# Kernel optimization log

Hardware: AMD Instinct MI355X
Metric: run time of the kernel (lower is better)

The kernel has to match this reference:

```python
import jax, jax.numpy as jnp
import numpy as np

# ---- static config (mirrors PointRend init kwargs) ----
H, W = 512, 512          # img_size
CH, CW = 128, 128        # coarse_size
FH, FW = 256, 256        # fine_size
CF = 256                 # fine_channels
NC = 3                   # num_classes (forced by MLP's hard-coded 259/131 channel counts)
NPTS = 2048              # N points
K_OVER = 3               # k oversampling
BELTA = 0.75
NUM_OVER = K_OVER * NPTS          # 6144
STEP1 = int(NPTS * BELTA)         # 1536 uncertain points
STEP2 = NPTS - STEP1              # 512 coverage points


def _xavier(key, c_out, c_in):
    std = (2.0 / (c_in + c_out)) ** 0.5
    return jax.random.normal(key, (c_out, c_in), jnp.float32) * std


def setup_inputs() -> dict:
    key = jax.random.key(0)
    k1, k2, k3, k4, k5, k6 = jax.random.split(key, 6)
    fine_grained = jax.random.normal(k1, (2, CF, FH, FW), jnp.float32)
    coarse_pre = jax.random.normal(k2, (2, NC, CH, CW), jnp.float32)
    # torch.randperm(H*W) done inside forward in the original; passed in for determinism
    random_1d_index = jax.random.permutation(k3, H * W).astype(jnp.int32)
    w1 = _xavier(k4, 256, CF + NC)   # conv1: 1x1, in=259, out=256, no bias
    w2 = _xavier(k5, 128, 256 + 3)   # conv2: in=259, out=128
    w3 = _xavier(k6, NC, 128 + 3)    # conv3: in=131, out=num_classes
    prelu_a = jnp.array(0.25, jnp.float32)  # shared single-param PReLU
    return dict(fine_grained=fine_grained, coarse_pre=coarse_pre,
                w1=w1, w2=w2, w3=w3, prelu_a=prelu_a,
                random_1d_index=random_1d_index)


def _bilinear(x, h, w):
    # matches nn.Upsample(mode='bilinear', align_corners=False)
    return jax.image.resize(x, (x.shape[0], x.shape[1], h, w), method="bilinear")


def _prelu(x, a):
    return jnp.where(x >= 0, x, a * x)


def _mlp(feat, w1, w2, w3, a):
    # feat: [B, N, C] -> channels-first [B, C, N]; BatchNorms in MLP are unused in forward.
    x = jnp.transpose(feat, (0, 2, 1))
    tail = x[:, -3:, :]  # last 3 channels appended to each layer's input
    l1 = _prelu(jnp.einsum('bcn,oc->bon', x, w1), a)
    l2 = _prelu(jnp.einsum('bcn,oc->bon', jnp.concatenate([l1, tail], 1), w2), a)
    return jnp.einsum('bcn,oc->bon', jnp.concatenate([l2, tail], 1), w3)  # [B, NC, N]


def reference(fine_grained, coarse_pre, w1, w2, w3, prelu_a, random_1d_index):
    B = fine_grained.shape[0]
    up_coarse_o = _bilinear(coarse_pre, H, W)            # [B, NC, H, W] logits
    up_coarse_sm = jax.nn.softmax(up_coarse_o, axis=1)   # softmax over classes
    up_fine = _bilinear(fine_grained, H, W)              # [B, CF, H, W]

    h_idx = random_1d_index // W
    w_idx = random_1d_index % W
    all_index = jnp.stack([h_idx, w_idx], axis=1)        # [H*W, 2]
    cand = all_index[:NUM_OVER]                          # oversampled candidates

    # vectorized replacement of the python loop: gather probs at candidates
    over_pre = up_coarse_sm[:, :, cand[:, 0], cand[:, 1]].transpose(0, 2, 1)  # [B, NUM_OVER, NC]
    top2, _ = jax.lax.top_k(over_pre, 2)
    uncertain = 1.0 - (top2[..., 0] - top2[..., 1])      # [B, NUM_OVER]
    _, u_idx = jax.lax.top_k(uncertain, STEP1)           # [B, STEP1]
    u_pts = cand[u_idx]                                  # [B, STEP1, 2]
    cov = jnp.broadcast_to(all_index[-STEP2:][None], (B, STEP2, 2))
    pts = jnp.concatenate([u_pts, cov], axis=1)          # [B, N, 2]

    # masked_select traverses the dense mask in row-major (h,w) order -> sort linear ids
    lin = pts[..., 0] * W + pts[..., 1]                  # [B, N]
    lin_sorted = jnp.sort(lin, axis=1)
    sh, sw = lin_sorted // W, lin_sorted % W
    bidx = jnp.arange(B)[:, None]
    sel_coarse = up_coarse_o[bidx, :, sh, sw]            # [B, N, NC] (pre-softmax feats)
    sel_fine = up_fine[bidx, :, sh, sw]                  # [B, N, CF]

    # faithful to torch: flat concat of the two masked_select outputs, then reshape
    feat = jnp.concatenate([sel_fine.reshape(-1), sel_coarse.reshape(-1)]).reshape(B, NPTS, -1)

    out = _mlp(feat, w1, w2, w3, prelu_a)                # [B, NC, N]
    mask = jnp.zeros((B, H, W), jnp.int32).at[bidx, pts[..., 0], pts[..., 1]].add(1)
    return out, mask
```

## Files before the change

### kernel.cpp

```cpp
#include <hip/hip_runtime.h>

#define NPTS 2048
#define NOVER 6144
#define STEP1 1536
#define STEP2 512
#define HW_TOT 262144

__device__ __forceinline__ float prelu_f(float x, float a) { return x >= 0.0f ? x : a * x; }

__device__ __forceinline__ void coarse_coords(int h, int w, float& fy, float& fx,
                                              int& y0, int& y1, int& x0, int& x1) {
  float sy = (h + 0.5f) * 0.25f - 0.5f;
  float sx = (w + 0.5f) * 0.25f - 0.5f;
  float yf = floorf(sy), xf = floorf(sx);
  fy = sy - yf; fx = sx - xf;
  int yi = (int)yf, xi = (int)xf;
  y0 = min(127, max(0, yi)); y1 = min(127, max(0, yi + 1));
  x0 = min(127, max(0, xi)); x1 = min(127, max(0, xi + 1));
}

__device__ __forceinline__ float coarse_sample(const float* __restrict__ ch, float fy, float fx,
                                               int y0, int y1, int x0, int x1) {
  float v00 = ch[(y0 << 7) + x0];
  float v01 = ch[(y0 << 7) + x1];
  float v10 = ch[(y1 << 7) + x0];
  float v11 = ch[(y1 << 7) + x1];
  return (1.0f - fy) * ((1.0f - fx) * v00 + fx * v01) + fy * ((1.0f - fx) * v10 + fx * v11);
}

__global__ __launch_bounds__(256) void pr_fill_v4(uint4* __restrict__ p) {
  p[blockIdx.x * 256 + threadIdx.x] = make_uint4(0u, 0u, 0u, 0u);
}

__global__ __launch_bounds__(256) void pr_wprep_v4(const float* __restrict__ w1,
                                                   const float* __restrict__ w2,
                                                   float* __restrict__ wT1,
                                                   float* __restrict__ wT2) {
  int gid = blockIdx.x * 256 + threadIdx.x;
  if (gid < 259 * 256) {
    int c = gid >> 8, o = gid & 255;
    wT1[c * 256 + o] = w1[o * 259 + c];
  } else {
    int g2 = gid - 259 * 256;
    if (g2 < 259 * 128) {
      int c = g2 >> 7, o = g2 & 127;
      wT2[c * 128 + o] = w2[o * 259 + c];
    }
  }
}

__global__ __launch_bounds__(256) void pr_uncert_v4(const float* __restrict__ coarse,
                                                    const int* __restrict__ ridx,
                                                    unsigned* __restrict__ keys) {
  int gid = blockIdx.x * 256 + threadIdx.x;
  if (gid >= 2 * NOVER) return;
  int b = gid / NOVER, i = gid - b * NOVER;
  int lin = ridx[i];
  int h = lin >> 9, w = lin & 511;
  float fy, fx; int y0, y1, x0, x1;
  coarse_coords(h, w, fy, fx, y0, y1, x0, x1);
  const float* cb = coarse + (((size_t)b * 3) << 14);
  float p0 = coarse_sample(cb, fy, fx, y0, y1, x0, x1);
  float p1 = coarse_sample(cb + (1 << 14), fy, fx, y0, y1, x0, x1);
  float p2 = coarse_sample(cb + (2 << 14), fy, fx, y0, y1, x0, x1);
  float m = fmaxf(p0, fmaxf(p1, p2));
  float e0 = expf(p0 - m), e1 = expf(p1 - m), e2 = expf(p2 - m);
  float s = e0 + e1 + e2;
  float q0 = e0 / s, q1 = e1 / s, q2 = e2 / s;
  float a0 = q0, a1 = q1, a2 = q2, tmp;
  if (a0 < a1) { tmp = a0; a0 = a1; a1 = tmp; }
  if (a1 < a2) { tmp = a1; a1 = a2; a2 = tmp; }
  if (a0 < a1) { tmp = a0; a0 = a1; a1 = tmp; }
  float u = 1.0f - (a0 - a1);
  keys[gid] = __float_as_uint(u);
}

__global__ __launch_bounds__(1024) void pr_topk_v4(const unsigned* __restrict__ keys,
                                                   const int* __restrict__ ridx,
                                                   int* __restrict__ lin_sorted,
                                                   float* __restrict__ mask) {
  __shared__ unsigned kv[NOVER];
  __shared__ unsigned bitmap[8192];
  __shared__ unsigned hist[256];
  __shared__ unsigned short tiebuf[NOVER];
  __shared__ unsigned scanbuf[16];
  __shared__ unsigned selinfo[2];
  __shared__ int tiecnt;
  const int b = blockIdx.x, t = threadIdx.x;
  const int lane = t & 63, wid = t >> 6;

  for (int i = t; i < NOVER; i += 1024) kv[i] = keys[b * NOVER + i];
  for (int i = t; i < 8192; i += 1024) bitmap[i] = 0u;
  if (t == 0) { selinfo[1] = STEP1; tiecnt = 0; }
  __syncthreads();

  unsigned prefix = 0u;
  for (int pass = 0; pass < 4; ++pass) {
    const int shift = 24 - 8 * pass;
    const unsigned maskHi = (pass == 0) ? 0u : (0xFFFFFFFFu << (shift + 8));
    for (int i = t; i < 256; i += 1024) hist[i] = 0u;
    __syncthreads();
    for (int i = t; i < NOVER; i += 1024) {
      unsigned k = kv[i];
      if ((k & maskHi) == prefix) atomicAdd(&hist[(k >> shift) & 255u], 1u);
    }
    __syncthreads();
    if (t < 64) {
      unsigned h0 = hist[t * 4], h1 = hist[t * 4 + 1], h2 = hist[t * 4 + 2], h3 = hist[t * 4 + 3];
      unsigned q = h0 + h1 + h2 + h3;
      unsigned s = q;
      for (int off = 1; off < 64; off <<= 1) {
        unsigned n = __shfl_down(s, off);
        if (t + off < 64) s += n;
      }
      unsigned exq = s - q;
      unsigned R = selinfo[1];
      unsigned se3 = exq, se2 = se3 + h3, se1 = se2 + h2, se0 = se1 + h1;
      if (se3 < R && R <= se3 + h3)      { selinfo[0] = prefix | ((unsigned)(t * 4 + 3) << shift); selinfo[1] = R - se3; }
      else if (se2 < R && R <= se2 + h2) { selinfo[0] = prefix | ((unsigned)(t * 4 + 2) << shift); selinfo[1] = R - se2; }
      else if (se1 < R && R <= se1 + h1) { selinfo[0] = prefix | ((unsigned)(t * 4 + 1) << shift); selinfo[1] = R - se1; }
      else if (se0 < R && R <= se0 + h0) { selinfo[0] = prefix | ((unsigned)(t * 4 + 0) << shift); selinfo[1] = R - se0; }
    }
    __syncthreads();
    prefix = selinfo[0];
  }
  const unsigned T = prefix;
  const int r = (int)selinfo[1];

  for (int i = t; i < NOVER; i += 1024) {
    unsigned k = kv[i];
    if (k > T) {
      int lin = ridx[i];
      mask[(size_t)b * HW_TOT + lin] = 1.0f;
      atomicOr(&bitmap[lin >> 5], 1u << (lin & 31));
    } else if (k == T) {
      int pos = atomicAdd(&tiecnt, 1);
      tiebuf[pos] = (unsigned short)i;
    }
  }
  for (int i = t; i < STEP2; i += 1024) {
    int lin = ridx[HW_TOT - STEP2 + i];
    mask[(size_t)b * HW_TOT + lin] = 1.0f;
    atomicOr(&bitmap[lin >> 5], 1u << (lin & 31));
  }
  __syncthreads();
  const int m = tiecnt;
  for (int j = t; j < m; j += 1024) {
    int idx = tiebuf[j];
    int rank = 0;
    for (int jj = 0; jj < m; ++jj) rank += (tiebuf[jj] < idx) ? 1 : 0;
    if (rank < r) {
      int lin = ridx[idx];
      mask[(size_t)b * HW_TOT + lin] = 1.0f;
      atomicOr(&bitmap[lin >> 5], 1u << (lin & 31));
    }
  }
  __syncthreads();

  unsigned mySum = 0;
#pragma unroll
  for (int q = 0; q < 8; ++q) mySum += __popc(bitmap[t * 8 + q]);
  unsigned v = mySum;
  for (int off = 1; off < 64; off <<= 1) {
    unsigned n = __shfl_up(v, off);
    if (lane >= off) v += n;
  }
  if (lane == 63) scanbuf[wid] = v;
  __syncthreads();
  if (t == 0) {
    unsigned run = 0;
    for (int w16 = 0; w16 < 16; ++w16) { unsigned tmp = scanbuf[w16]; scanbuf[w16] = run; run += tmp; }
  }
  __syncthreads();
  unsigned pos = (v - mySum) + scanbuf[wid];
  for (int q = 0; q < 8; ++q) {
    unsigned word = bitmap[t * 8 + q];
    int basebit = (t * 8 + q) << 5;
    while (word) {
      int bit = __ffs(word) - 1;
      word &= word - 1;
      lin_sorted[b * NPTS + pos++] = basebit + bit;
    }
  }
}

__global__ __launch_bounds__(512) void pr_mlp_v6(const float* __restrict__ fine,
                                                 const float* __restrict__ coarse,
                                                 const float* __restrict__ wT1,
                                                 const float* __restrict__ wT2,
                                                 const float* __restrict__ w3,
                                                 const float* __restrict__ pa,
                                                 const int* __restrict__ lin_sorted,
                                                 float* __restrict__ out) {
  __shared__ __align__(16) float wbuf[2][8192];
  __shared__ __align__(16) float xs[259][16];
  __shared__ __align__(16) float l1p[16][260];
  __shared__ __align__(16) float l2p[16][132];
  const int t = threadIdx.x;
  const int g0 = blockIdx.x * 16;
  const float a = pa[0];

  const int ob1 = (t & 63) * 4;
  const int pq1 = (t >> 6) * 2;
  const int ob2 = (t & 31) * 4;
  const int pt2 = t >> 5;

  float4 t1[3], t2[3];
#pragma unroll
  for (int i = 0; i < 3; ++i) {
    t1[i] = *(const float4*)&wT1[(256 + i) * 256 + ob1];
    t2[i] = *(const float4*)&wT2[(256 + i) * 128 + ob2];
  }
  float4 st[4];
#pragma unroll
  for (int j = 0; j < 4; ++j) st[j] = *(const float4*)&wT1[(j * 512 + t) * 4];

  for (int task = t; task < 259 * 16; task += 512) {
    int c = task >> 4, p = task & 15;
    int g = g0 + p;
    int j = g * 259 + c;
    float v;
    if (j < 1048576) {
      int nsrc = j >> 8, ch = j & 255;
      int bs = nsrc >> 11;
      int lin = lin_sorted[nsrc];
      int h = lin >> 9, w = lin & 511;
      float sy = (h + 0.5f) * 0.5f - 0.5f;
      float sx = (w + 0.5f) * 0.5f - 0.5f;
      float yf = floorf(sy), xf = floorf(sx);
      float fy = sy - yf, fx = sx - xf;
      int yi = (int)yf, xi = (int)xf;
      int y0 = min(255, max(0, yi)), y1 = min(255, max(0, yi + 1));
      int x0 = min(255, max(0, xi)), x1 = min(255, max(0, xi + 1));
      const float* base = fine + (((size_t)(bs * 256 + ch)) << 16);
      float v00 = base[(y0 << 8) + x0];
      float v01 = base[(y0 << 8) + x1];
      float v10 = base[(y1 << 8) + x0];
      float v11 = base[(y1 << 8) + x1];
      v = (1.0f - fy) * ((1.0f - fx) * v00 + fx * v01) + fy * ((1.0f - fx) * v10 + fx * v11);
    } else {
      int jj = j - 1048576;
      int nsrc = jj / 3;
      int kk = jj - nsrc * 3;
      int bs = nsrc >> 11;
      int lin = lin_sorted[nsrc];
      int h = lin >> 9, w = lin & 511;
      float fy, fx; int y0, y1, x0, x1;
      coarse_coords(h, w, fy, fx, y0, y1, x0, x1);
      v = coarse_sample(coarse + (((size_t)bs * 3 + kk) << 14), fy, fx, y0, y1, x0, x1);
    }
    xs[c][p] = v;
  }
#pragma unroll
  for (int j = 0; j < 4; ++j) *(float4*)&wbuf[0][(j * 512 + t) * 4] = st[j];
  __syncthreads();

  float acc1[4][2];
#pragma unroll
  for (int i = 0; i < 4; ++i) { acc1[i][0] = 0.0f; acc1[i][1] = 0.0f; }
  float acc2[4] = {0.0f, 0.0f, 0.0f, 0.0f};

  for (int k = 0; k < 12; ++k) {
    const int cur = k & 1;
    if (k < 11) {
      const float* src;
      if (k < 7)       src = wT1 + (k + 1) * 8192;
      else if (k == 7) src = wT2;
      else             src = wT2 + (k - 7) * 8192;
#pragma unroll
      for (int j = 0; j < 4; ++j) st[j] = *(const float4*)&src[(j * 512 + t) * 4];
    }

    if (k < 8) {
      const float* w = wbuf[cur];
      const int c0 = k * 32;
#pragma unroll 8
      for (int cl = 0; cl < 32; ++cl) {
        const float4 wv = *(const float4*)&w[cl * 256 + ob1];
        const float2 xv = *(const float2*)&xs[c0 + cl][pq1];
        acc1[0][0] = fmaf(wv.x, xv.x, acc1[0][0]); acc1[0][1] = fmaf(wv.x, xv.y, acc1[0][1]);
        acc1[1][0] = fmaf(wv.y, xv.x, acc1[1][0]); acc1[1][1] = fmaf(wv.y, xv.y, acc1[1][1]);
        acc1[2][0] = fmaf(wv.z, xv.x, acc1[2][0]); acc1[2][1] = fmaf(wv.z, xv.y, acc1[2][1]);
        acc1[3][0] = fmaf(wv.w, xv.x, acc1[3][0]); acc1[3][1] = fmaf(wv.w, xv.y, acc1[3][1]);
      }
      if (k == 7) {
#pragma unroll
        for (int i = 0; i < 3; ++i) {
          const float2 xv = *(const float2*)&xs[256 + i][pq1];
          acc1[0][0] = fmaf(t1[i].x, xv.x, acc1[0][0]); acc1[0][1] = fmaf(t1[i].x, xv.y, acc1[0][1]);
          acc1[1][0] = fmaf(t1[i].y, xv.x, acc1[1][0]); acc1[1][1] = fmaf(t1[i].y, xv.y, acc1[1][1]);
          acc1[2][0] = fmaf(t1[i].z, xv.x, acc1[2][0]); acc1[2][1] = fmaf(t1[i].z, xv.y, acc1[2][1]);
          acc1[3][0] = fmaf(t1[i].w, xv.x, acc1[3][0]); acc1[3][1] = fmaf(t1[i].w, xv.y, acc1[3][1]);
        }
#pragma unroll
        for (int q = 0; q < 2; ++q) {
          float4 o;
          o.x = prelu_f(acc1[0][q], a);
          o.y = prelu_f(acc1[1][q], a);
          o.z = prelu_f(acc1[2][q], a);
          o.w = prelu_f(acc1[3][q], a);
          *(float4*)&l1p[pq1 + q][ob1] = o;
        }
      }
    } else {
      const float* w = wbuf[cur];
      const int c0 = (k - 8) * 64;
#pragma unroll 4
      for (int cl = 0; cl < 64; cl += 4) {
        const float4 xv = *(const float4*)&l1p[pt2][c0 + cl];
        const float4 w0 = *(const float4*)&w[(cl + 0) * 128 + ob2];
        const float4 w1v = *(const float4*)&w[(cl + 1) * 128 + ob2];
        const float4 w2v = *(const float4*)&w[(cl + 2) * 128 + ob2];
        const float4 w3v = *(const float4*)&w[(cl + 3) * 128 + ob2];
        acc2[0] = fmaf(w0.x, xv.x, acc2[0]); acc2[1] = fmaf(w0.y, xv.x, acc2[1]);
        acc2[2] = fmaf(w0.z, xv.x, acc2[2]); acc2[3] = fmaf(w0.w, xv.x, acc2[3]);
        acc2[0] = fmaf(w1v.x, xv.y, acc2[0]); acc2[1] = fmaf(w1v.y, xv.y, acc2[1]);
        acc2[2] = fmaf(w1v.z, xv.y, acc2[2]); acc2[3] = fmaf(w1v.w, xv.y, acc2[3]);
        acc2[0] = fmaf(w2v.x, xv.z, acc2[0]); acc2[1] = fmaf(w2v.y, xv.z, acc2[1]);
        acc2[2] = fmaf(w2v.z, xv.z, acc2[2]); acc2[3] = fmaf(w2v.w, xv.z, acc2[3]);
        acc2[0] = fmaf(w3v.x, xv.w, acc2[0]); acc2[1] = fmaf(w3v.y, xv.w, acc2[1]);
        acc2[2] = fmaf(w3v.z, xv.w, acc2[2]); acc2[3] = fmaf(w3v.w, xv.w, acc2[3]);
      }
      if (k == 11) {
#pragma unroll
        for (int i = 0; i < 3; ++i) {
          const float x0 = xs[256 + i][pt2];
          acc2[0] = fmaf(t2[i].x, x0, acc2[0]); acc2[1] = fmaf(t2[i].y, x0, acc2[1]);
          acc2[2] = fmaf(t2[i].z, x0, acc2[2]); acc2[3] = fmaf(t2[i].w, x0, acc2[3]);
        }
        float4 o;
        o.x = prelu_f(acc2[0], a);
        o.y = prelu_f(acc2[1], a);
        o.z = prelu_f(acc2[2], a);
        o.w = prelu_f(acc2[3], a);
        *(float4*)&l2p[pt2][ob2] = o;
      }
    }

    if (k < 11) {
#pragma unroll
      for (int j = 0; j < 4; ++j) *(float4*)&wbuf[cur ^ 1][(j * 512 + t) * 4] = st[j];
    }
    __syncthreads();
  }

  if (t < 48) {
    const int o3 = t % 3, p = t / 3;
    const float* wr = w3 + o3 * 131;
    float s = 0.0f;
#pragma unroll 4
    for (int c = 0; c < 128; ++c) s = fmaf(wr[c], l2p[p][c], s);
#pragma unroll
    for (int kk = 0; kk < 3; ++kk) s = fmaf(wr[128 + kk], xs[256 + kk][p], s);
    const int g = g0 + p;
    out[((g >> 11) * 3 + o3) * 2048 + (g & 2047)] = s;
  }
}

extern "C" void kernel_launch(void* const* d_in, const int* in_sizes, int n_in,
                              void* d_out, int out_size, void* d_ws, size_t ws_size,
                              hipStream_t stream) {
  const float* fine   = (const float*)d_in[0];
  const float* coarse = (const float*)d_in[1];
  const float* w1     = (const float*)d_in[2];
  const float* w2     = (const float*)d_in[3];
  const float* w3     = (const float*)d_in[4];
  const float* pa     = (const float*)d_in[5];
  const int*   ridx   = (const int*)d_in[6];

  float* out  = (float*)d_out;
  float* mask = out + 2 * 3 * 2048;

  char* ws = (char*)d_ws;
  int*      lin_sorted = (int*)ws;
  float*    wT1  = (float*)(ws + 16384);
  float*    wT2  = (float*)(ws + 16384 + 265216);
  unsigned* keys = (unsigned*)(ws + 16384 + 265216 + 132608);

  pr_fill_v4<<<512, 256, 0, stream>>>((uint4*)mask);
  pr_wprep_v4<<<389, 256, 0, stream>>>(w1, w2, wT1, wT2);
  pr_uncert_v4<<<48, 256, 0, stream>>>(coarse, ridx, keys);
  pr_topk_v4<<<2, 1024, 0, stream>>>(keys, ridx, lin_sorted, mask);
  pr_mlp_v6<<<256, 512, 0, stream>>>(fine, coarse, wT1, wT2, w3, pa, lin_sorted, out);
}
```

Baseline: 274.1 us.

## Split bilinear feature gather into a separate wide kernel before MLP

Moves the bilinear sampling of fine and coarse features out of the MLP kernel into its own kernel, launched with 4144 blocks of 256 threads and one thread per feature element. It writes the features to a workspace buffer, and the MLP kernel then just loads them into shared memory. The gather also reads float4 row segments and picks the needed lanes instead of doing four scalar loads. This spreads the latency-bound random gathers across many more waves than the 256-block MLP grid could run, at the cost of an extra launch and about 4 MB of global write and read traffic.

New measurement: 278.1 us. Within noise of the previous version (+1.5%).

```diff
diff --git a/kernel.cpp b/kernel.cpp
--- a/kernel.cpp
+++ b/kernel.cpp
@@ -184,14 +184,63 @@
   }
 }
 
-__global__ __launch_bounds__(512) void pr_mlp_v6(const float* __restrict__ fine,
-                                                 const float* __restrict__ coarse,
-                                                 const float* __restrict__ wT1,
-                                                 const float* __restrict__ wT2,
-                                                 const float* __restrict__ w3,
-                                                 const float* __restrict__ pa,
-                                                 const int* __restrict__ lin_sorted,
-                                                 float* __restrict__ out) {
+__device__ __forceinline__ float pick4(float4 v, int r) {
+  return r == 0 ? v.x : (r == 1 ? v.y : (r == 2 ? v.z : v.w));
+}
+
+__global__ __launch_bounds__(256) void pr_gather_v8(const float* __restrict__ fine,
+                                                    const float* __restrict__ coarse,
+                                                    const int* __restrict__ lin_sorted,
+                                                    float* __restrict__ featbuf) {
+  const int tid = blockIdx.x * 256 + threadIdx.x;
+  if (tid < 1048576) {
+    const int s = tid >> 8, ch = tid & 255;
+    const int bs = s >> 11;
+    const int lin = lin_sorted[s];
+    const int h = lin >> 9, w = lin & 511;
+    float sy = (h + 0.5f) * 0.5f - 0.5f;
+    float sx = (w + 0.5f) * 0.5f - 0.5f;
+    float yf = floorf(sy), xf = floorf(sx);
+    float fy = sy - yf, fx = sx - xf;
+    int yi = (int)yf, xi = (int)xf;
+    int y0 = min(255, max(0, yi)), y1 = min(255, max(0, yi + 1));
+    int x0 = min(255, max(0, xi)), x1 = min(255, max(0, xi + 1));
+    const float* base = fine + (((size_t)(bs * 256 + ch)) << 16);
+    const float4* row0 = (const float4*)(base + (y0 << 8));
+    const float4* row1 = (const float4*)(base + (y1 << 8));
+    const int q0 = x0 >> 2, q1 = x1 >> 2;
+    const int r0 = x0 & 3, r1 = x1 & 3;
+    float4 A = row0[q0];
+    float4 B = row1[q0];
+    float4 C, D;
+    if (q1 != q0) {
+      C = row0[q1];
+      D = row1[q1];
+    } else {
+      C = A; D = B;
+    }
+    float v00 = pick4(A, r0), v10 = pick4(B, r0);
+    float v01 = pick4(C, r1), v11 = pick4(D, r1);
+    featbuf[tid] = (1.0f - fy) * ((1.0f - fx) * v00 + fx * v01)
+                 + fy * ((1.0f - fx) * v10 + fx * v11);
+  } else {
+    const int u = tid - 1048576;
+    const int nsrc = u / 3, kk = u - nsrc * 3;
+    const int bs = nsrc >> 11;
+    const int lin = lin_sorted[nsrc];
+    const int h = lin >> 9, w = lin & 511;
+    float fy, fx; int y0, y1, x0, x1;
+    coarse_coords(h, w, fy, fx, y0, y1, x0, x1);
+    featbuf[tid] = coarse_sample(coarse + (((size_t)bs * 3 + kk) << 14), fy, fx, y0, y1, x0, x1);
+  }
+}
+
+__global__ __launch_bounds__(512) void pr_mlpc_v8(const float* __restrict__ featbuf,
+                                                  const float* __restrict__ wT1,
+                                                  const float* __restrict__ wT2,
+                                                  const float* __restrict__ w3,
+                                                  const float* __restrict__ pa,
+                                                  float* __restrict__ out) {
   __shared__ __align__(16) float wbuf[2][8192];
   __shared__ __align__(16) float xs[259][16];
   __shared__ __align__(16) float l1p[16][260];
@@ -215,41 +264,12 @@
 #pragma unroll
   for (int j = 0; j < 4; ++j) st[j] = *(const float4*)&wT1[(j * 512 + t) * 4];
 
-  for (int task = t; task < 259 * 16; task += 512) {
-    int c = task >> 4, p = task & 15;
-    int g = g0 + p;
-    int j = g * 259 + c;
-    float v;
-    if (j < 1048576) {
-      int nsrc = j >> 8, ch = j & 255;
-      int bs = nsrc >> 11;
-      int lin = lin_sorted[nsrc];
-      int h = lin >> 9, w = lin & 511;
-      float sy = (h + 0.5f) * 0.5f - 0.5f;
-      float sx = (w + 0.5f) * 0.5f - 0.5f;
-      float yf = floorf(sy), xf = floorf(sx);
-      float fy = sy - yf, fx = sx - xf;
-      int yi = (int)yf, xi = (int)xf;
-      int y0 = min(255, max(0, yi)), y1 = min(255, max(0, yi + 1));
-      int x0 = min(255, max(0, xi)), x1 = min(255, max(0, xi + 1));
-      const float* base = fine + (((size_t)(bs * 256 + ch)) << 16);
-      float v00 = base[(y0 << 8) + x0];
-      float v01 = base[(y0 << 8) + x1];
-      float v10 = base[(y1 << 8) + x0];
-      float v11 = base[(y1 << 8) + x1];
-      v = (1.0f - fy) * ((1.0f - fx) * v00 + fx * v01) + fy * ((1.0f - fx) * v10 + fx * v11);
-    } else {
-      int jj = j - 1048576;
-      int nsrc = jj / 3;
-      int kk = jj - nsrc * 3;
-      int bs = nsrc >> 11;
-      int lin = lin_sorted[nsrc];
-      int h = lin >> 9, w = lin & 511;
-      float fy, fx; int y0, y1, x0, x1;
-      coarse_coords(h, w, fy, fx, y0, y1, x0, x1);
-      v = coarse_sample(coarse + (((size_t)bs * 3 + kk) << 14), fy, fx, y0, y1, x0, x1);
-    }
-    xs[c][p] = v;
+  {
+    const int jbase = g0 * 259;
+    for (int jj = t; jj < 259 * 16; jj += 512) {
+      int p = jj / 259, c = jj - p * 259;
+      xs[c][p] = featbuf[jbase + jj];
+    }
   }
 #pragma unroll
   for (int j = 0; j < 4; ++j) *(float4*)&wbuf[0][(j * 512 + t) * 4] = st[j];
@@ -373,13 +393,15 @@
 
   char* ws = (char*)d_ws;
   int*      lin_sorted = (int*)ws;
-  float*    wT1  = (float*)(ws + 16384);
-  float*    wT2  = (float*)(ws + 16384 + 265216);
-  unsigned* keys = (unsigned*)(ws + 16384 + 265216 + 132608);
+  float*    wT1     = (float*)(ws + 16384);
+  float*    wT2     = (float*)(ws + 281600);
+  unsigned* keys    = (unsigned*)(ws + 414208);
+  float*    featbuf = (float*)(ws + 463360);
 
   pr_fill_v4<<<512, 256, 0, stream>>>((uint4*)mask);
   pr_wprep_v4<<<389, 256, 0, stream>>>(w1, w2, wT1, wT2);
   pr_uncert_v4<<<48, 256, 0, stream>>>(coarse, ridx, keys);
   pr_topk_v4<<<2, 1024, 0, stream>>>(keys, ridx, lin_sorted, mask);
-  pr_mlp_v6<<<256, 512, 0, stream>>>(fine, coarse, wT1, wT2, w3, pa, lin_sorted, out);
-}
+  pr_gather_v8<<<4144, 256, 0, stream>>>(fine, coarse, lin_sorted, featbuf);
+  pr_mlpc_v8<<<256, 512, 0, stream>>>(featbuf, wT1, wT2, w3, pa, out);
+}
```

## Split bilinear gather into separate coalesced kernel and fuse mask fill with uncertainty

Applied to the files above, without the earlier changes.

Bilinear sampling of fine and coarse features moves out of the MLP kernel into a dedicated gather kernel. It is laid out channel-major so each thread handles one (channel, point) pair and the kernel runs across many blocks. The MLP kernel then reads the precomputed values from a workspace buffer. The mask zero-fill is folded into the uncertainty kernel to save a launch, and the layer-1 thread-to-output mapping is reorganised. This adds a few MB of workspace traffic and an extra launch in exchange for better parallelism in the gather.

After: 280.3 us. +2.3%, slower.

```diff
diff --git a/kernel.cpp b/kernel.cpp
--- a/kernel.cpp
+++ b/kernel.cpp
@@ -28,31 +28,16 @@
   return (1.0f - fy) * ((1.0f - fx) * v00 + fx * v01) + fy * ((1.0f - fx) * v10 + fx * v11);
 }
 
-__global__ __launch_bounds__(256) void pr_fill_v4(uint4* __restrict__ p) {
-  p[blockIdx.x * 256 + threadIdx.x] = make_uint4(0u, 0u, 0u, 0u);
-}
-
-__global__ __launch_bounds__(256) void pr_wprep_v4(const float* __restrict__ w1,
-                                                   const float* __restrict__ w2,
-                                                   float* __restrict__ wT1,
-                                                   float* __restrict__ wT2) {
-  int gid = blockIdx.x * 256 + threadIdx.x;
-  if (gid < 259 * 256) {
-    int c = gid >> 8, o = gid & 255;
-    wT1[c * 256 + o] = w1[o * 259 + c];
-  } else {
-    int g2 = gid - 259 * 256;
-    if (g2 < 259 * 128) {
-      int c = g2 >> 7, o = g2 & 127;
-      wT2[c * 128 + o] = w2[o * 259 + c];
-    }
-  }
-}
-
-__global__ __launch_bounds__(256) void pr_uncert_v4(const float* __restrict__ coarse,
-                                                    const int* __restrict__ ridx,
-                                                    unsigned* __restrict__ keys) {
-  int gid = blockIdx.x * 256 + threadIdx.x;
+__global__ __launch_bounds__(256) void pr_uncfill_v9(uint4* __restrict__ mask4,
+                                                     const float* __restrict__ coarse,
+                                                     const int* __restrict__ ridx,
+                                                     unsigned* __restrict__ keys) {
+  const int bb = blockIdx.x;
+  if (bb < 512) {
+    mask4[bb * 256 + threadIdx.x] = make_uint4(0u, 0u, 0u, 0u);
+    return;
+  }
+  int gid = (bb - 512) * 256 + threadIdx.x;
   if (gid >= 2 * NOVER) return;
   int b = gid / NOVER, i = gid - b * NOVER;
   int lin = ridx[i];
@@ -75,6 +60,23 @@
   keys[gid] = __float_as_uint(u);
 }
 
+__global__ __launch_bounds__(256) void pr_wprep_v4(const float* __restrict__ w1,
+                                                   const float* __restrict__ w2,
+                                                   float* __restrict__ wT1,
+                                                   float* __restrict__ wT2) {
+  int gid = blockIdx.x * 256 + threadIdx.x;
+  if (gid < 259 * 256) {
+    int c = gid >> 8, o = gid & 255;
+    wT1[c * 256 + o] = w1[o * 259 + c];
+  } else {
+    int g2 = gid - 259 * 256;
+    if (g2 < 259 * 128) {
+      int c = g2 >> 7, o = g2 & 127;
+      wT2[c * 128 + o] = w2[o * 259 + c];
+    }
+  }
+}
+
 __global__ __launch_bounds__(1024) void pr_topk_v4(const unsigned* __restrict__ keys,
                                                    const int* __restrict__ ridx,
                                                    int* __restrict__ lin_sorted,
@@ -184,24 +186,61 @@
   }
 }
 
-__global__ __launch_bounds__(512) void pr_mlp_v6(const float* __restrict__ fine,
-                                                 const float* __restrict__ coarse,
-                                                 const float* __restrict__ wT1,
-                                                 const float* __restrict__ wT2,
-                                                 const float* __restrict__ w3,
-                                                 const float* __restrict__ pa,
-                                                 const int* __restrict__ lin_sorted,
-                                                 float* __restrict__ out) {
+__global__ __launch_bounds__(256) void pr_gather_v9(const float* __restrict__ fine,
+                                                    const float* __restrict__ coarse,
+                                                    const int* __restrict__ lin_sorted,
+                                                    float* __restrict__ fv,
+                                                    float* __restrict__ cv) {
+  const int tid = blockIdx.x * 256 + threadIdx.x;
+  if (tid < 1048576) {
+    const int s = tid & 4095, ch = tid >> 12;
+    const int bs = s >> 11;
+    const int lin = lin_sorted[s];
+    const int h = lin >> 9, w = lin & 511;
+    float sy = (h + 0.5f) * 0.5f - 0.5f;
+    float sx = (w + 0.5f) * 0.5f - 0.5f;
+    float yf = floorf(sy), xf = floorf(sx);
+    float fy = sy - yf, fx = sx - xf;
+    int yi = (int)yf, xi = (int)xf;
+    int y0 = min(255, max(0, yi)), y1 = min(255, max(0, yi + 1));
+    int x0 = min(255, max(0, xi)), x1 = min(255, max(0, xi + 1));
+    const float* base = fine + (((size_t)(bs * 256 + ch)) << 16);
+    float v00 = base[(y0 << 8) + x0];
+    float v01 = base[(y0 << 8) + x1];
+    float v10 = base[(y1 << 8) + x0];
+    float v11 = base[(y1 << 8) + x1];
+    fv[tid] = (1.0f - fy) * ((1.0f - fx) * v00 + fx * v01)
+            + fy * ((1.0f - fx) * v10 + fx * v11);
+  } else {
+    const int u = tid - 1048576;
+    const int s = u & 4095, kk = u >> 12;
+    const int bs = s >> 11;
+    const int lin = lin_sorted[s];
+    const int h = lin >> 9, w = lin & 511;
+    float fy, fx; int y0, y1, x0, x1;
+    coarse_coords(h, w, fy, fx, y0, y1, x0, x1);
+    cv[u] = coarse_sample(coarse + (((size_t)bs * 3 + kk) << 14), fy, fx, y0, y1, x0, x1);
+  }
+}
+
+__global__ __launch_bounds__(512) void pr_mlpc_v10(const float* __restrict__ fv,
+                                                   const float* __restrict__ cv,
+                                                   const float* __restrict__ wT1,
+                                                   const float* __restrict__ wT2,
+                                                   const float* __restrict__ w3,
+                                                   const float* __restrict__ pa,
+                                                   float* __restrict__ out) {
   __shared__ __align__(16) float wbuf[2][8192];
   __shared__ __align__(16) float xs[259][16];
   __shared__ __align__(16) float l1p[16][260];
   __shared__ __align__(16) float l2p[16][132];
   const int t = threadIdx.x;
+  const int lane = t & 63, wid = t >> 6;
   const int g0 = blockIdx.x * 16;
   const float a = pa[0];
 
-  const int ob1 = (t & 63) * 4;
-  const int pq1 = (t >> 6) * 2;
+  const int ob1 = ((wid & 3) << 6) + ((lane & 15) << 2);
+  const int pp1 = ((wid >> 2) << 3) + ((lane >> 4) << 1);
   const int ob2 = (t & 31) * 4;
   const int pt2 = t >> 5;
 
@@ -217,37 +256,14 @@
 
   for (int task = t; task < 259 * 16; task += 512) {
     int c = task >> 4, p = task & 15;
-    int g = g0 + p;
-    int j = g * 259 + c;
+    int j = (g0 + p) * 259 + c;
     float v;
     if (j < 1048576) {
-      int nsrc = j >> 8, ch = j & 255;
-      int bs = nsrc >> 11;
-      int lin = lin_sorted[nsrc];
-      int h = lin >> 9, w = lin & 511;
-      float sy = (h + 0.5f) * 0.5f - 0.5f;
-      float sx = (w + 0.5f) * 0.5f - 0.5f;
-      float yf = floorf(sy), xf = floorf(sx);
-      float fy = sy - yf, fx = sx - xf;
-      int yi = (int)yf, xi = (int)xf;
-      int y0 = min(255, max(0, yi)), y1 = min(255, max(0, yi + 1));
-      int x0 = min(255, max(0, xi)), x1 = min(255, max(0, xi + 1));
-      const float* base = fine + (((size_t)(bs * 256 + ch)) << 16);
-      float v00 = base[(y0 << 8) + x0];
-      float v01 = base[(y0 << 8) + x1];
-      float v10 = base[(y1 << 8) + x0];
-      float v11 = base[(y1 << 8) + x1];
-      v = (1.0f - fy) * ((1.0f - fx) * v00 + fx * v01) + fy * ((1.0f - fx) * v10 + fx * v11);
+      v = fv[(j & 255) * 4096 + (j >> 8)];
     } else {
       int jj = j - 1048576;
-      int nsrc = jj / 3;
-      int kk = jj - nsrc * 3;
-      int bs = nsrc >> 11;
-      int lin = lin_sorted[nsrc];
-      int h = lin >> 9, w = lin & 511;
-      float fy, fx; int y0, y1, x0, x1;
-      coarse_coords(h, w, fy, fx, y0, y1, x0, x1);
-      v = coarse_sample(coarse + (((size_t)bs * 3 + kk) << 14), fy, fx, y0, y1, x0, x1);
+      int nsrc = jj / 3, kk = jj - nsrc * 3;
+      v = cv[kk * 4096 + nsrc];
     }
     xs[c][p] = v;
   }
@@ -277,7 +293,7 @@
 #pragma unroll 8
       for (int cl = 0; cl < 32; ++cl) {
         const float4 wv = *(const float4*)&w[cl * 256 + ob1];
-        const float2 xv = *(const float2*)&xs[c0 + cl][pq1];
+        const float2 xv = *(const float2*)&xs[c0 + cl][pp1];
         acc1[0][0] = fmaf(wv.x, xv.x, acc1[0][0]); acc1[0][1] = fmaf(wv.x, xv.y, acc1[0][1]);
         acc1[1][0] = fmaf(wv.y, xv.x, acc1[1][0]); acc1[1][1] = fmaf(wv.y, xv.y, acc1[1][1]);
         acc1[2][0] = fmaf(wv.z, xv.x, acc1[2][0]); acc1[2][1] = fmaf(wv.z, xv.y, acc1[2][1]);
@@ -286,7 +302,7 @@
       if (k == 7) {
 #pragma unroll
         for (int i = 0; i < 3; ++i) {
-          const float2 xv = *(const float2*)&xs[256 + i][pq1];
+          const float2 xv = *(const float2*)&xs[256 + i][pp1];
           acc1[0][0] = fmaf(t1[i].x, xv.x, acc1[0][0]); acc1[0][1] = fmaf(t1[i].x, xv.y, acc1[0][1]);
           acc1[1][0] = fmaf(t1[i].y, xv.x, acc1[1][0]); acc1[1][1] = fmaf(t1[i].y, xv.y, acc1[1][1]);
           acc1[2][0] = fmaf(t1[i].z, xv.x, acc1[2][0]); acc1[2][1] = fmaf(t1[i].z, xv.y, acc1[2][1]);
@@ -299,7 +315,7 @@
           o.y = prelu_f(acc1[1][q], a);
           o.z = prelu_f(acc1[2][q], a);
           o.w = prelu_f(acc1[3][q], a);
-          *(float4*)&l1p[pq1 + q][ob1] = o;
+          *(float4*)&l1p[pp1 + q][ob1] = o;
         }
       }
     } else {
@@ -374,12 +390,14 @@
   char* ws = (char*)d_ws;
   int*      lin_sorted = (int*)ws;
   float*    wT1  = (float*)(ws + 16384);
-  float*    wT2  = (float*)(ws + 16384 + 265216);
-  unsigned* keys = (unsigned*)(ws + 16384 + 265216 + 132608);
-
-  pr_fill_v4<<<512, 256, 0, stream>>>((uint4*)mask);
+  float*    wT2  = (float*)(ws + 281600);
+  unsigned* keys = (unsigned*)(ws + 414208);
+  float*    fv   = (float*)(ws + 463360);
+  float*    cv   = (float*)(ws + 4657664);
+
+  pr_uncfill_v9<<<560, 256, 0, stream>>>((uint4*)mask, coarse, ridx, keys);
   pr_wprep_v4<<<389, 256, 0, stream>>>(w1, w2, wT1, wT2);
-  pr_uncert_v4<<<48, 256, 0, stream>>>(coarse, ridx, keys);
   pr_topk_v4<<<2, 1024, 0, stream>>>(keys, ridx, lin_sorted, mask);
-  pr_mlp_v6<<<256, 512, 0, stream>>>(fine, coarse, wT1, wT2, w3, pa, lin_sorted, out);
-}
+  pr_gather_v9<<<4144, 256, 0, stream>>>(fine, coarse, lin_sorted, fv, cv);
+  pr_mlpc_v10<<<256, 512, 0, stream>>>(fv, cv, wT1, wT2, w3, pa, out);
+}
```
